# Performance work log

Measured on AMD Instinct MI355X. Metric: run time of the kernel, lower is better.

## Reference

```python
import jax, jax.numpy as jnp
import numpy as np

SIGMA = 0.002  # TreeEnergyLoss default; edge weight = exp(-||df||^2 / sigma)


def bilinear_resize(x, oh, ow):
    """F.interpolate(mode='bilinear', align_corners=False), no antialias. x: [B,C,H,W]."""
    B, C, H, W = x.shape
    if (H, W) == (oh, ow):
        return x
    def coords(o, n):
        s = (jnp.arange(o, dtype=jnp.float32) + 0.5) * (n / o) - 0.5
        s = jnp.clip(s, 0.0, n - 1.0)
        lo = jnp.floor(s).astype(jnp.int32)
        hi = jnp.minimum(lo + 1, n - 1)
        return lo, hi, s - lo.astype(jnp.float32)
    r0, r1, rf = coords(oh, H)
    c0, c1, cf = coords(ow, W)
    xr = x[:, :, r0, :] * (1.0 - rf)[None, None, :, None] + x[:, :, r1, :] * rf[None, None, :, None]
    return xr[:, :, :, c0] * (1.0 - cf) + xr[:, :, :, c1] * cf


def nearest_resize(x, oh, ow):
    B, C, H, W = x.shape
    if (H, W) == (oh, ow):
        return x
    ri = jnp.floor(jnp.arange(oh) * (H / oh)).astype(jnp.int32)
    ci = jnp.floor(jnp.arange(ow) * (W / ow)).astype(jnp.int32)
    return x[:, :, ri, :][:, :, :, ci]


def _mst_bfs_np(embed, H, W):
    """Kruskal MST on the 4-connected pixel grid (edge cost = squared L2 feature
    distance, as in MinimumSpanningTree(TreeFilter2D.norm2_distance)), then BFS
    order from vertex 0. embed: np [C,H,W]. Returns (sorted_index, sorted_parent)
    where sorted_parent is the BFS position of each vertex's parent."""
    V = H * W
    idx = np.arange(V).reshape(H, W)
    eu = np.concatenate([idx[:-1, :].ravel(), idx[:, :-1].ravel()])
    ev = np.concatenate([idx[1:, :].ravel(), idx[:, 1:].ravel()])
    f = embed.reshape(embed.shape[0], V)
    cost = ((f[:, eu] - f[:, ev]) ** 2).sum(0)
    parent = np.arange(V)
    def find(x):
        root = x
        while parent[root] != root:
            root = parent[root]
        while parent[x] != root:
            parent[x], x = root, parent[x]
        return root
    nbr = [[] for _ in range(V)]
    cnt = 0
    for e in np.argsort(cost, kind='stable'):
        u, v = int(eu[e]), int(ev[e])
        ru, rv = find(u), find(v)
        if ru != rv:
            parent[ru] = rv
            nbr[u].append(v)
            nbr[v].append(u)
            cnt += 1
            if cnt == V - 1:
                break
    sorted_index = np.empty(V, np.int32)
    sorted_parent = np.empty(V, np.int32)
    visited = np.zeros(V, bool)
    sorted_index[0] = 0; sorted_parent[0] = 0; visited[0] = True
    head, tail = 0, 1
    while head < tail:
        u = int(sorted_index[head])
        for v in nbr[u]:
            if not visited[v]:
                visited[v] = True
                sorted_index[tail] = v
                sorted_parent[tail] = head
                tail += 1
        head += 1
    return sorted_index, sorted_parent


def build_trees(embed):
    """embed: [B,C,H,W]. Host-side MST+BFS per batch element (torch.no_grad in original)."""
    e = np.asarray(jax.lax.stop_gradient(embed), dtype=np.float64)
    B, C, H, W = e.shape
    si, sp = zip(*[_mst_bfs_np(e[b], H, W) for b in range(B)])
    return jnp.asarray(np.stack(si)), jnp.asarray(np.stack(sp))


def _tree_filter_single(f, embed, sorted_index, sorted_parent):
    """Normalized tree filter: out_i = sum_j W_ij f_j / sum_j W_ij with
    W_ij = prod of exp(-||de||^2/sigma) along the unique tree path i->j.
    Computed exactly via bottom-up aggregation + top-down propagation in BFS order.
    f: [C,V], embed: [Ce,V]."""
    C, V = f.shape
    fs = f[:, sorted_index]                        # [C,V] features in BFS order
    es = embed[:, sorted_index]
    d = ((es - es[:, sorted_parent]) ** 2).sum(0)  # [V]; d[0]=0 (root self edge)
    w = jnp.exp(-d / SIGMA)                        # edge weight to parent
    # bottom-up: children have larger BFS index, so reverse order is valid.
    # extra ones-row carries the normalizer Z through the same recursion.
    S0 = jnp.concatenate([fs, jnp.ones((1, V), fs.dtype)], axis=0)
    def up(S, j):
        return S.at[:, sorted_parent[j]].add(w[j] * S[:, j]), None
    S, _ = jax.lax.scan(up, S0, jnp.arange(V - 1, 0, -1))
    # top-down: A_root = S_root; A_j = S_j + w_j * (A_parent - w_j * S_j)
    def down(A, j):
        p = sorted_parent[j]
        return A.at[:, j].set(S[:, j] + w[j] * (A[:, p] - w[j] * S[:, j])), None
    A0 = jnp.zeros_like(S).at[:, 0].set(S[:, 0])
    A, _ = jax.lax.scan(down, A0, jnp.arange(1, V))
    out_sorted = A[:C] / A[C]
    return jnp.zeros_like(f).at[:, sorted_index].set(out_sorted)


def tree_filter(feature, embed, si, sp):
    B, C, h, w = feature.shape
    out = jax.vmap(_tree_filter_single)(
        feature.reshape(B, C, h * w),
        embed.reshape(B, embed.shape[1], h * w), si, sp)
    return out.reshape(B, C, h, w)


def setup_inputs():
    key = jax.random.key(0)
    k1, k2, k3, k4 = jax.random.split(key, 4)
    preds = jax.random.normal(k1, (8, 21, 80, 80), jnp.float32)
    # scaled so exp(-||df||^2 / 0.002) gives non-degenerate edge weights
    low_feats = jax.random.uniform(k2, (8, 3, 80, 80), jnp.float32) * 0.02
    high_feats = jax.random.normal(k3, (8, 256, 80, 80), jnp.float32) * 0.002
    unlabeled_ROIs = jax.random.randint(k4, (8, 80, 80), 0, 2, dtype=jnp.int32)
    return {"preds": preds, "low_feats": low_feats,
            "high_feats": high_feats, "unlabeled_ROIs": unlabeled_ROIs}


def reference(preds, low_feats, high_feats, unlabeled_ROIs):
    B, C, h, w = preds.shape
    low = bilinear_resize(low_feats, h, w)  # under torch.no_grad in original
    roi = nearest_resize(unlabeled_ROIs[:, None].astype(jnp.float32), h, w)
    si_l, sp_l = build_trees(low)
    si_h, sp_h = build_trees(high_feats)
    prob = jax.nn.softmax(preds, axis=1)
    AS = tree_filter(prob, jax.lax.stop_gradient(low), si_l, sp_l)  # low-level tree
    AS = tree_filter(AS, high_feats, si_h, sp_h)                    # high-level tree
    N = roi.sum()
    loss = (roi * jnp.abs(prob - AS)).sum()
    return jnp.where(N > 0, loss / N, jnp.zeros((), preds.dtype))  # weight = 1.0
```

## Files before the change

kernel.cpp:

```cpp
#include <hip/hip_runtime.h>

#define BB 8
#define CP 21
#define CF 22
#define CLOW 3
#define CHIGH 256
#define WW 80
#define VV 6400
#define EVERT 6320
#define EE 12640
#define TT 16
#define SIGMA_F 0.002f
#define ROOT 3240

#define NE (VV - 1)
#define NA (2 * NE)
#define NILA 0xFFFFu
#define NB 200

__device__ __forceinline__ void edge_uv(int e, int& u, int& v) {
  if (e < EVERT) { u = e; v = e + WW; }
  else { int e2 = e - EVERT; int r = e2 / (WW - 1); int c = e2 - r * (WW - 1); u = r * WW + c; v = u + 1; }
}

__global__ void k_softmax(const float* __restrict__ preds, float* __restrict__ prob) {
  int i = blockIdx.x * blockDim.x + threadIdx.x;
  if (i >= BB * VV) return;
  int b = i / VV, v = i - b * VV;
  const float* p = preds + (size_t)b * CP * VV + v;
  float m = -1e30f;
  #pragma unroll
  for (int c = 0; c < CP; c++) m = fmaxf(m, p[c * VV]);
  float e[CP], s = 0.f;
  #pragma unroll
  for (int c = 0; c < CP; c++) { float x = expf(p[c * VV] - m); e[c] = x; s += x; }
  float inv = 1.f / s;
  float* o = prob + (size_t)b * CP * VV + v;
  #pragma unroll
  for (int c = 0; c < CP; c++) o[c * VV] = e[c] * inv;
}

__global__ void k_edgekey(const float* __restrict__ low, const float* __restrict__ high,
                          unsigned long long* __restrict__ ekey) {
  int i = blockIdx.x * blockDim.x + threadIdx.x;
  if (i >= TT * EE) return;
  int t = i / EE, e = i - t * EE;
  int u, v; edge_uv(e, u, v);
  double acc = 0.0;
  if (t < BB) {
    const float* emb = low + (size_t)t * CLOW * VV;
    for (int c = 0; c < CLOW; c++) { double d = (double)emb[c * VV + u] - (double)emb[c * VV + v]; acc += d * d; }
  } else {
    const float* emb = high + (size_t)(t - BB) * CHIGH * VV;
    for (int c = 0; c < CHIGH; c++) { double d = (double)emb[c * VV + u] - (double)emb[c * VV + v]; acc += d * d; }
  }
  unsigned long long bits = (unsigned long long)__double_as_longlong(acc);
  ekey[i] = (bits & ~0x3FFFULL) | (unsigned long long)e;
}

__global__ __launch_bounds__(1024) void k_msttree(const unsigned long long* __restrict__ ekey,
    int* __restrict__ mstU, int* __restrict__ mstV,
    int* __restrict__ ordG, int* __restrict__ spG,
    int* __restrict__ lpG, int* __restrict__ nlevG, float* __restrict__ wvp) {
  int t = blockIdx.x;
  const unsigned long long* key = ekey + (size_t)t * EE;
  int* mu = mstU + t * VV;
  int* mv = mstV + t * VV;
  int tid = threadIdx.x;
  const int nt = 1024;
  int lane = tid & 63, wid = tid >> 6;

  __shared__ alignas(16) char arena[144384];
  __shared__ int lasts, spackU, spackW, scenter, smaxd, changed, cnt, necnt;

  int* comp = (int*)(arena + 0);
  unsigned long long* bst = (unsigned long long*)(arena + 25600);
  unsigned short* tgtS = (unsigned short*)(arena + 76800);
  unsigned short* el0 = (unsigned short*)(arena + 89600);
  unsigned short* el1 = (unsigned short*)(arena + 114880);

  char* buf = arena;
  int* deg = (int*)(buf + 0);
  int* off = (int*)(buf + 25600);
  unsigned short* adjA = (unsigned short*)(buf + 51208);
  unsigned short* succ = (unsigned short*)(buf + 102408);
  int* pk0 = (int*)(buf + 0);
  int* pk1 = (int*)(buf + 51208);
  unsigned short* r_a = (unsigned short*)(buf + 102408);
  short* H = (short*)(buf + 51208);
  unsigned short* depthR = (unsigned short*)(buf + 76808);
  unsigned short* firstK = (unsigned short*)(buf + 89608);
  short* prefmin = (short*)(buf + 0);
  short* sufmin  = (short*)(buf + 25600);
  unsigned short* distU = (unsigned short*)(buf + 76808);
  unsigned short* parentS = (unsigned short*)(buf + 76808);
  int* lev = (int*)(buf + 0);
  int* cur = (int*)(buf + 25604);
  unsigned short* ordS = (unsigned short*)(buf + 51208);
  unsigned short* posS = (unsigned short*)(buf + 64008);
  int* part = (int*)(buf + 128016);
  short* tbl = (short*)(buf + 128272);
  unsigned short* dbuf2 = (unsigned short*)(buf + 131472);

  auto blockScanEx = [&](int s) -> int {
    int x = s;
    #pragma unroll
    for (int d = 1; d < 64; d <<= 1) { int o = __shfl_up(x, d); if (lane >= d) x += o; }
    if (lane == 63) part[wid] = x;
    __syncthreads();
    if (wid == 0) {
      int y = (lane < 16) ? part[lane] : 0;
      #pragma unroll
      for (int d = 1; d < 16; d <<= 1) { int o = __shfl_up(y, d); if (lane >= d) y += o; }
      if (lane < 16) part[lane] = y;
    }
    __syncthreads();
    int base = (wid > 0) ? part[wid - 1] : 0;
    return base + (x - s);
  };

  for (int v = tid; v < VV; v += nt) comp[v] = v;
  for (int e = tid; e < EE; e += nt) el0[e] = (unsigned short)e;
  if (tid == 0) cnt = 0;
  __syncthreads();
  {
    unsigned short* els = el0;
    unsigned short* eld = el1;
    int ecnt = EE;
    for (int round = 0; round < 48 && ecnt > 0; round++) {
      for (int v = tid; v < VV; v += nt) bst[v] = ~0ULL;
      if (tid == 0) { changed = 0; necnt = 0; }
      __syncthreads();
      for (int j = tid; j < ecnt; j += nt) {
        int e = els[j];
        int u, v; edge_uv(e, u, v);
        int cu = comp[u], cv = comp[v];
        if (cu != cv) { unsigned long long k = key[e]; atomicMin(&bst[cu], k); atomicMin(&bst[cv], k); }
      }
      __syncthreads();
      for (int c = tid; c < VV; c += nt) {
        unsigned short tg = (unsigned short)NILA;
        if (comp[c] == c) {
          unsigned long long k = bst[c];
          if (k != ~0ULL) {
            int e = (int)(k & 0x3FFFULL);
            int u, v; edge_uv(e, u, v);
            int cu = comp[u], cv = comp[v];
            tg = (unsigned short)((cu == c) ? cv : cu);
          }
        }
        tgtS[c] = tg;
      }
      __syncthreads();
      for (int c = tid; c < VV; c += nt) {
        int o = tgtS[c];
        if (o == (int)NILA) continue;
        unsigned long long k = bst[c];
        if (bst[o] == k && c < o) continue;
        comp[c] = o;
        int slot = atomicAdd(&cnt, 1);
        int e = (int)(k & 0x3FFFULL);
        int u, v; edge_uv(e, u, v);
        mu[slot] = u; mv[slot] = v;
        changed = 1;
      }
      __syncthreads();
      if (!changed) break;
      for (int v = tid; v < VV; v += nt) {
        int c = comp[v];
        int c2 = comp[c];
        if (c2 != c) {
          int r0 = c2;
          while (true) { int n = comp[r0]; if (n == r0) break; r0 = n; }
          comp[v] = r0;
        }
      }
      __syncthreads();
      for (int j = tid; j < ecnt; j += nt) {
        int e = els[j];
        int u, v; edge_uv(e, u, v);
        if (comp[u] != comp[v]) { int s = atomicAdd(&necnt, 1); eld[s] = (unsigned short)e; }
      }
      __syncthreads();
      ecnt = necnt;
      __syncthreads();
      unsigned short* tp = els; els = eld; eld = tp;
    }
  }
  __threadfence();
  __syncthreads();

  for (int v = tid; v < VV; v += nt) deg[v] = 0;
  __syncthreads();
  for (int e = tid; e < NE; e += nt) { atomicAdd(&deg[mu[e]], 1); atomicAdd(&deg[mv[e]], 1); }
  __syncthreads();
  {
    const int SCH = 7;
    int base = tid * SCH;
    int s = 0;
    #pragma unroll
    for (int k = 0; k < SCH; k++) { int v = base + k; if (v < VV) s += deg[v]; }
    int ex = blockScanEx(s);
    #pragma unroll
    for (int k = 0; k < SCH; k++) { int v = base + k; if (v < VV) { off[v] = ex; ex += deg[v]; } }
    if (tid == 1023) off[VV] = ex;
  }
  __syncthreads();
  for (int v = tid; v < VV; v += nt) deg[v] = off[v];
  __syncthreads();
  for (int e = tid; e < NE; e += nt) {
    int u = mu[e], v = mv[e];
    adjA[atomicAdd(&deg[u], 1)] = (unsigned short)(2 * e);
    adjA[atomicAdd(&deg[v], 1)] = (unsigned short)(2 * e + 1);
  }
  __syncthreads();
  for (int v = tid; v < VV; v += nt) {
    int b0 = off[v], dv = off[v + 1] - b0;
    for (int k = 0; k < dv; k++) {
      unsigned short a = adjA[b0 + k];
      unsigned short b = adjA[b0 + ((k + 1 == dv) ? 0 : k + 1)];
      succ[a ^ 1] = b;
    }
  }
  if (tid == 0) lasts = adjA[off[ROOT] + (off[ROOT + 1] - off[ROOT]) - 1] ^ 1;
  __syncthreads();
  if (tid == 0) succ[lasts] = (unsigned short)NILA;
  __syncthreads();
  for (int a = tid; a < NA; a += nt) {
    unsigned int n = succ[a];
    pk0[a] = ((n == NILA ? 0 : 1) << 16) | (int)n;
  }
  __syncthreads();
  {
    int* px = pk0;
    int* py = pk1;
    for (int rd = 0; rd < 14; rd++) {
      for (int a = tid; a < NA; a += nt) {
        int cur_ = px[a];
        int n = cur_ & 0xFFFF;
        if (n != (int)NILA) {
          int o = px[n];
          cur_ = (((cur_ >> 16) + (o >> 16)) << 16) | (o & 0xFFFF);
        }
        py[a] = cur_;
      }
      __syncthreads();
      int* tp = px; px = py; py = tp;
    }
    for (int a = tid; a < NA; a += nt) r_a[a] = (unsigned short)(pk0[a] >> 16);
  }
  __syncthreads();
  for (int a = tid; a < NA; a += nt) {
    int pa = NA - 1 - (int)r_a[a];
    int pb = NA - 1 - (int)r_a[a ^ 1];
    H[pa] = (pa < pb) ? (short)1 : (short)-1;
  }
  __syncthreads();
  {
    const int SCH = 13;
    int base = tid * SCH;
    int lim = base + SCH; if (lim > NA) lim = NA;
    int s = 0;
    for (int j = base; j < lim; j++) s += H[j];
    int run = blockScanEx(s);
    for (int j = base; j < lim; j++) { run += H[j]; H[j] = (short)run; }
  }
  __syncthreads();
  if (tid == 0) { spackU = 0; smaxd = 0; scenter = 0x7FFFFFFF; }
  __syncthreads();
  for (int a = tid; a < NA; a += nt) {
    int pa = NA - 1 - (int)r_a[a];
    int pb = NA - 1 - (int)r_a[a ^ 1];
    if (pa < pb) {
      int e = a >> 1;
      int head = (a & 1) ? mu[e] : mv[e];
      depthR[head] = (unsigned short)H[pa];
      firstK[head] = (unsigned short)(pa + 1);
    }
  }
  if (tid == 0) { depthR[ROOT] = 0; firstK[ROOT] = 0; }
  __syncthreads();
  {
    int loc = 0;
    for (int v = tid; v < VV; v += nt) { int p = ((int)depthR[v] << 13) | v; if (p > loc) loc = p; }
    #pragma unroll
    for (int d = 32; d > 0; d >>= 1) { int o = __shfl_down(loc, d); if (o > loc) loc = o; }
    if (lane == 0) atomicMax(&spackU, loc);
  }
  __syncthreads();
  {
    for (int seg = wid; seg < NB; seg += 16) {
      int p = seg * 64 + lane;
      int h = (p < NA) ? (int)H[p] : 32767;
      int hp = h;
      #pragma unroll
      for (int d = 1; d < 64; d <<= 1) { int o = __shfl_up(hp, d); if (lane >= d && o < hp) hp = o; }
      prefmin[p] = (short)hp;
      int hs = h;
      #pragma unroll
      for (int d = 1; d < 64; d <<= 1) { int o = __shfl_down(hs, d); if (lane + d < 64 && o < hs) hs = o; }
      sufmin[p] = (short)hs;
      if (lane == 0) tbl[seg] = (short)hs;
    }
  }
  __syncthreads();
  for (int k = 1; k < 8; k++) {
    short vv_ = 0;
    if (tid < NB) {
      int o = tid + (1 << (k - 1));
      short a = tbl[(k - 1) * NB + tid];
      short b2 = (o < NB) ? tbl[(k - 1) * NB + o] : (short)32767;
      vv_ = (a < b2) ? a : b2;
    }
    __syncthreads();
    if (tid < NB) tbl[k * NB + tid] = vv_;
    __syncthreads();
  }
  auto distq = [&](int K1, int K2) -> int {
    if (K1 == K2) return 0;
    int l = (K1 < K2 ? K1 : K2) - 1;
    int r = (K1 > K2 ? K1 : K2) - 1;
    int m = 32767;
    int l0 = l < 0 ? 0 : l;
    int bl = l0 >> 6, br = r >> 6;
    if (bl == br) {
      for (int p = l0; p <= r; p++) { int h = H[p]; if (h < m) m = h; }
    } else {
      int a = sufmin[l0], b2 = prefmin[r];
      m = a < b2 ? a : b2;
      int lo = bl + 1, hi = br - 1;
      if (lo <= hi) {
        int L = hi - lo + 1;
        int k = 31 - __builtin_clz(L);
        int c1 = tbl[k * NB + lo];
        int c2 = tbl[k * NB + hi - (1 << k) + 1];
        if (c1 < m) m = c1;
        if (c2 < m) m = c2;
      }
    }
    if (l < 0 && 0 < m) m = 0;
    int h1 = (K1 == 0) ? 0 : (int)H[K1 - 1];
    int h2 = (K2 == 0) ? 0 : (int)H[K2 - 1];
    return h1 + h2 - 2 * m;
  };
  int u = spackU & 0x1FFF;
  int Ku = firstK[u];
  if (tid == 0) spackW = 0;
  __syncthreads();
  {
    int loc = 0;
    for (int v = tid; v < VV; v += nt) {
      int d = distq(Ku, firstK[v]);
      distU[v] = (unsigned short)d;
      int p = (d << 13) | v;
      if (p > loc) loc = p;
    }
    #pragma unroll
    for (int d = 32; d > 0; d >>= 1) { int o = __shfl_down(loc, d); if (o > loc) loc = o; }
    if (lane == 0) atomicMax(&spackW, loc);
  }
  __syncthreads();
  int D = spackW >> 13;
  int w = spackW & 0x1FFF;
  int Kw = firstK[w];
  for (int v = tid; v < VV; v += nt) dbuf2[v] = (unsigned short)distq(Kw, firstK[v]);
  __syncthreads();
  {
    int half = D >> 1;
    for (int v = tid; v < VV; v += nt) {
      if ((int)distU[v] == half && (int)distU[v] + (int)dbuf2[v] == D) atomicMin(&scenter, v);
    }
  }
  __syncthreads();
  int cvert = (scenter == 0x7FFFFFFF) ? ROOT : scenter;
  int Kc = firstK[cvert];
  __syncthreads();
  {
    int loc = 0;
    for (int v = tid; v < VV; v += nt) {
      int d = distq(Kc, firstK[v]);
      dbuf2[v] = (unsigned short)d;
      if (d > loc) loc = d;
    }
    #pragma unroll
    for (int d = 32; d > 0; d >>= 1) { int o = __shfl_down(loc, d); if (o > loc) loc = o; }
    if (lane == 0) atomicMax(&smaxd, loc);
  }
  __syncthreads();
  int maxd = smaxd;
  int sTil = Kc;
  for (int a = tid; a < NA; a += nt) {
    int pa = NA - 1 - (int)r_a[a];
    int pb = NA - 1 - (int)r_a[a ^ 1];
    int pa2 = pa - sTil; if (pa2 < 0) pa2 += NA;
    int pb2 = pb - sTil; if (pb2 < 0) pb2 += NA;
    if (pa2 < pb2) {
      int e = a >> 1;
      int head = (a & 1) ? mu[e] : mv[e];
      int tail = (a & 1) ? mv[e] : mu[e];
      parentS[head] = (unsigned short)tail;
    }
  }
  if (tid == 0) parentS[cvert] = (unsigned short)cvert;
  __syncthreads();
  for (int d = tid; d <= VV; d += nt) lev[d] = 0;
  __syncthreads();
  for (int v = tid; v < VV; v += nt) atomicAdd(&lev[dbuf2[v]], 1);
  __syncthreads();
  {
    const int SCH = 7;
    int base = tid * SCH;
    int s = 0;
    #pragma unroll
    for (int k = 0; k < SCH; k++) { int d = base + k; if (d <= VV) s += lev[d]; }
    int ex = blockScanEx(s);
    #pragma unroll
    for (int k = 0; k < SCH; k++) {
      int d = base + k;
      if (d <= VV) {
        int st = ex;
        ex += lev[d];
        if (d < VV) cur[d] = st;
        lpG[t * (VV + 1) + d] = st;
      }
    }
  }
  __syncthreads();
  for (int v = tid; v < VV; v += nt) {
    int d = dbuf2[v];
    int slot = atomicAdd(&cur[d], 1);
    ordS[slot] = (unsigned short)v;
    posS[v] = (unsigned short)slot;
  }
  __syncthreads();
  for (int j = tid; j < VV; j += nt) {
    int v = ordS[j];
    int pv = parentS[v];
    ordG[t * VV + j] = v;
    spG[t * VV + j] = posS[pv];
    float wout;
    if (v == pv) {
      wout = 1.0f;
    } else {
      int a = v < pv ? v : pv;
      int diff = v < pv ? pv - v : v - pv;
      int e;
      if (diff == WW) e = a;
      else { int r = a / WW, c = a - r * WW; e = EVERT + r * (WW - 1) + c; }
      unsigned long long k = key[e];
      double cost = __longlong_as_double((long long)(k & ~0x3FFFULL));
      wout = expf(-(float)cost / SIGMA_F);
    }
    wvp[t * VV + j] = wout;
  }
  if (tid == 0) nlevG[t] = maxd + 1;
}

__global__ __launch_bounds__(512) void k_filter_pc(const float* __restrict__ Fsrc, float* __restrict__ Araw,
    const float* __restrict__ wvp, const int* __restrict__ ordG, const int* __restrict__ spG,
    const int* __restrict__ lpG, const int* __restrict__ nlevG, int treeBase) {
  int blk = blockIdx.x;
  int b = blk / CF, ch = blk - b * CF;
  int t = treeBase + b;
  __shared__ alignas(16) char arena[140816];
  float2* ab0 = (float2*)(arena);
  float2* ab1 = (float2*)(arena + 51200);
  float*  S   = (float*)(arena + 51200);
  float*  w   = (float*)(arena + 76800);
  unsigned short* sp0 = (unsigned short*)(arena + 102400);
  unsigned short* sp1 = (unsigned short*)(arena + 115200);
  unsigned short* lpS = (unsigned short*)(arena + 128000);
  const int* ord = ordG + t * VV;
  const int* spt = spG + t * VV;
  const float* wsrc = wvp + t * VV;
  const int* lp = lpG + t * (VV + 1);
  int tid = threadIdx.x;
  const int nt = 512;
  int NL = nlevG[t];
  for (int j = tid; j <= NL; j += nt) lpS[j] = (unsigned short)lp[j];
  const bool norm_in = (treeBase != 0);
  for (int j = tid; j < VV; j += nt) {
    sp0[j] = (unsigned short)spt[j];
    w[j] = wsrc[j];
    float val;
    if (ch < CP) {
      int v = ord[j];
      if (!norm_in) val = Fsrc[((size_t)b * CP + ch) * VV + v];
      else          val = Fsrc[((size_t)b * CF + ch) * VV + v] / Fsrc[((size_t)b * CF + CP) * VV + v];
    } else val = 1.0f;
    S[j] = val;
  }
  __syncthreads();
  if (tid < 64) {
    int s1 = lpS[NL];
    int s0 = lpS[NL - 1];
    for (int l = NL - 1; l >= 1; l--) {
      int s0n = (l > 1) ? (int)lpS[l - 1] : 0;
      for (int j = s0 + tid; j < s1; j += 64) {
        atomicAdd(&S[sp0[j]], w[j] * S[j]);
      }
      asm volatile("s_waitcnt lgkmcnt(0)" ::: "memory");
      __builtin_amdgcn_sched_barrier(0);
      s1 = s0; s0 = s0n;
    }
  }
  __syncthreads();
  for (int j = tid; j < VV; j += nt) {
    float wv = w[j];
    float a = (j == 0) ? 0.f : wv;
    float bv = (j == 0) ? S[0] : S[j] * (1.f - wv * wv);
    ab0[j] = make_float2(a, bv);
  }
  __syncthreads();
  int rounds = 0;
  { int d = 1; while (d < NL) { d <<= 1; rounds++; } }
  float2 *abs_ = ab0, *abd_ = ab1;
  unsigned short *ps_ = sp0, *pd_ = sp1;
  for (int r = 0; r < rounds; r++) {
    for (int j = tid; j < VV; j += nt) {
      float2 m = abs_[j];
      int p = ps_[j];
      float2 o = m;
      int pn = p;
      if (m.x != 0.f) {
        float2 mp = abs_[p];
        pn = ps_[p];
        o.x = m.x * mp.x;
        o.y = fmaf(m.x, mp.y, m.y);
      }
      abd_[j] = o;
      pd_[j] = (unsigned short)pn;
    }
    __syncthreads();
    float2* tf = abs_; abs_ = abd_; abd_ = tf;
    unsigned short* tu = ps_; ps_ = pd_; pd_ = tu;
  }
  float* Ob = Araw + ((size_t)b * CF + ch) * VV;
  for (int j = tid; j < VV; j += nt) Ob[ord[j]] = abs_[j].y;
}

__global__ void k_loss(const float* __restrict__ prob, const float* __restrict__ Araw2,
                       const int* __restrict__ roi, double* __restrict__ acc) {
  int i = blockIdx.x * blockDim.x + threadIdx.x;
  int tid = threadIdx.x;
  double s = 0.0, n = 0.0;
  if (i < BB * VV) {
    int b = i / VV, v = i - b * VV;
    if (roi[i] != 0) {
      n = 1.0;
      const float* pb = prob + (size_t)b * CP * VV + v;
      const float* ab = Araw2 + (size_t)b * CF * VV + v;
      float inv = 1.0f / ab[CP * VV];
      float ls = 0.f;
      #pragma unroll
      for (int c = 0; c < CP; c++) ls += fabsf(pb[c * VV] - ab[c * VV] * inv);
      s = (double)ls;
    }
  }
  __shared__ double rs[256], rn[256];
  rs[tid] = s; rn[tid] = n;
  __syncthreads();
  for (int d = 128; d > 0; d >>= 1) {
    if (tid < d) { rs[tid] += rs[tid + d]; rn[tid] += rn[tid + d]; }
    __syncthreads();
  }
  if (tid == 0) { atomicAdd(&acc[0], rs[0]); atomicAdd(&acc[1], rn[0]); }
}

__global__ void k_finalize(const double* __restrict__ acc, float* __restrict__ out) {
  out[0] = (acc[1] > 0.0) ? (float)(acc[0] / acc[1]) : 0.0f;
}

extern "C" void kernel_launch(void* const* d_in, const int* in_sizes, int n_in,
                              void* d_out, int out_size, void* d_ws, size_t ws_size,
                              hipStream_t stream) {
  const float* preds = (const float*)d_in[0];
  const float* low   = (const float*)d_in[1];
  const float* high  = (const float*)d_in[2];
  const int*   roi   = (const int*)d_in[3];
  float* out = (float*)d_out;

  char* w = (char*)d_ws;
  size_t off = 0;
  auto alloc = [&](size_t bytes) -> void* {
    void* p = w + off;
    off += (bytes + 255) & ~(size_t)255;
    return p;
  };
  float* prob  = (float*)alloc((size_t)BB * CP * VV * 4);
  float* Araw1 = (float*)alloc((size_t)BB * CF * VV * 4);
  float* Araw2 = (float*)alloc((size_t)BB * CF * VV * 4);
  unsigned long long* ekey = (unsigned long long*)alloc((size_t)TT * EE * 8);
  int* mstU = (int*)alloc((size_t)TT * VV * 4);
  int* mstV = (int*)alloc((size_t)TT * VV * 4);
  int* ordG = (int*)alloc((size_t)TT * VV * 4);
  int* spG  = (int*)alloc((size_t)TT * VV * 4);
  int* lpG  = (int*)alloc((size_t)TT * (VV + 1) * 4);
  int* nlev = (int*)alloc((size_t)TT * 4);
  float* wvp = (float*)alloc((size_t)TT * VV * 4);
  double* acc = (double*)alloc(16);

  hipMemsetAsync(acc, 0, 16, stream);

  k_softmax<<<(BB * VV + 255) / 256, 256, 0, stream>>>(preds, prob);
  k_edgekey<<<(TT * EE + 255) / 256, 256, 0, stream>>>(low, high, ekey);
  k_msttree<<<TT, 1024, 0, stream>>>(ekey, mstU, mstV, ordG, spG, lpG, nlev, wvp);
  k_filter_pc<<<BB * CF, 512, 0, stream>>>(prob,  Araw1, wvp, ordG, spG, lpG, nlev, 0);
  k_filter_pc<<<BB * CF, 512, 0, stream>>>(Araw1, Araw2, wvp, ordG, spG, lpG, nlev, BB);
  k_loss<<<(BB * VV + 255) / 256, 256, 0, stream>>>(prob, Araw2, roi, acc);
  k_finalize<<<1, 1, 0, stream>>>(acc, out);
}
```

Measured before the change: 301.1 us.

## Fold softmax into MST kernel, fuse finalize into loss, widen filter blocks

Softmax now runs as extra blocks of the MST kernel launch, so it uses the CUs left idle by the 16 MST blocks. The finalize kernel is removed: the last k_loss block, found with an atomic done-counter, writes the result. The filter kernel goes from 512 to 1024 threads per block to parallelise the per-level scans. This saves two launches and fills idle hardware, at the cost of more register pressure from the 1024-thread launch bound and extra code inside the MST kernel.

```diff
diff --git a/kernel.cpp b/kernel.cpp
--- a/kernel.cpp
+++ b/kernel.cpp
@@ -17,27 +17,11 @@
 #define NA (2 * NE)
 #define NILA 0xFFFFu
 #define NB 200
+#define SMB ((BB * VV + 255) / 256)
 
 __device__ __forceinline__ void edge_uv(int e, int& u, int& v) {
   if (e < EVERT) { u = e; v = e + WW; }
   else { int e2 = e - EVERT; int r = e2 / (WW - 1); int c = e2 - r * (WW - 1); u = r * WW + c; v = u + 1; }
-}
-
-__global__ void k_softmax(const float* __restrict__ preds, float* __restrict__ prob) {
-  int i = blockIdx.x * blockDim.x + threadIdx.x;
-  if (i >= BB * VV) return;
-  int b = i / VV, v = i - b * VV;
-  const float* p = preds + (size_t)b * CP * VV + v;
-  float m = -1e30f;
-  #pragma unroll
-  for (int c = 0; c < CP; c++) m = fmaxf(m, p[c * VV]);
-  float e[CP], s = 0.f;
-  #pragma unroll
-  for (int c = 0; c < CP; c++) { float x = expf(p[c * VV] - m); e[c] = x; s += x; }
-  float inv = 1.f / s;
-  float* o = prob + (size_t)b * CP * VV + v;
-  #pragma unroll
-  for (int c = 0; c < CP; c++) o[c * VV] = e[c] * inv;
 }
 
 __global__ void k_edgekey(const float* __restrict__ low, const float* __restrict__ high,
@@ -61,7 +45,26 @@
 __global__ __launch_bounds__(1024) void k_msttree(const unsigned long long* __restrict__ ekey,
     int* __restrict__ mstU, int* __restrict__ mstV,
     int* __restrict__ ordG, int* __restrict__ spG,
-    int* __restrict__ lpG, int* __restrict__ nlevG, float* __restrict__ wvp) {
+    int* __restrict__ lpG, int* __restrict__ nlevG, float* __restrict__ wvp,
+    const float* __restrict__ preds, float* __restrict__ prob) {
+  if (blockIdx.x >= TT) {
+    int i = (blockIdx.x - TT) * 1024 + threadIdx.x;
+    if (i < BB * VV) {
+      int b = i / VV, v = i - b * VV;
+      const float* p = preds + (size_t)b * CP * VV + v;
+      float m = -1e30f;
+      #pragma unroll
+      for (int c = 0; c < CP; c++) m = fmaxf(m, p[c * VV]);
+      float e[CP], s = 0.f;
+      #pragma unroll
+      for (int c = 0; c < CP; c++) { float x = expf(p[c * VV] - m); e[c] = x; s += x; }
+      float inv = 1.f / s;
+      float* o = prob + (size_t)b * CP * VV + v;
+      #pragma unroll
+      for (int c = 0; c < CP; c++) o[c * VV] = e[c] * inv;
+    }
+    return;
+  }
   int t = blockIdx.x;
   const unsigned long long* key = ekey + (size_t)t * EE;
   int* mu = mstU + t * VV;
@@ -456,7 +459,7 @@
   if (tid == 0) nlevG[t] = maxd + 1;
 }
 
-__global__ __launch_bounds__(512) void k_filter_pc(const float* __restrict__ Fsrc, float* __restrict__ Araw,
+__global__ __launch_bounds__(1024) void k_filter_pc(const float* __restrict__ Fsrc, float* __restrict__ Araw,
     const float* __restrict__ wvp, const int* __restrict__ ordG, const int* __restrict__ spG,
     const int* __restrict__ lpG, const int* __restrict__ nlevG, int treeBase) {
   int blk = blockIdx.x;
@@ -475,7 +478,7 @@
   const float* wsrc = wvp + t * VV;
   const int* lp = lpG + t * (VV + 1);
   int tid = threadIdx.x;
-  const int nt = 512;
+  const int nt = 1024;
   int NL = nlevG[t];
   for (int j = tid; j <= NL; j += nt) lpS[j] = (unsigned short)lp[j];
   const bool norm_in = (treeBase != 0);
@@ -540,7 +543,8 @@
 }
 
 __global__ void k_loss(const float* __restrict__ prob, const float* __restrict__ Araw2,
-                       const int* __restrict__ roi, double* __restrict__ acc) {
+                       const int* __restrict__ roi, double* __restrict__ acc,
+                       unsigned int* __restrict__ done, float* __restrict__ out) {
   int i = blockIdx.x * blockDim.x + threadIdx.x;
   int tid = threadIdx.x;
   double s = 0.0, n = 0.0;
@@ -558,17 +562,26 @@
     }
   }
   __shared__ double rs[256], rn[256];
+  __shared__ bool amLast;
   rs[tid] = s; rn[tid] = n;
   __syncthreads();
   for (int d = 128; d > 0; d >>= 1) {
     if (tid < d) { rs[tid] += rs[tid + d]; rn[tid] += rn[tid + d]; }
     __syncthreads();
   }
-  if (tid == 0) { atomicAdd(&acc[0], rs[0]); atomicAdd(&acc[1], rn[0]); }
-}
-
-__global__ void k_finalize(const double* __restrict__ acc, float* __restrict__ out) {
-  out[0] = (acc[1] > 0.0) ? (float)(acc[0] / acc[1]) : 0.0f;
+  if (tid == 0) {
+    atomicAdd(&acc[0], rs[0]);
+    atomicAdd(&acc[1], rn[0]);
+    __threadfence();
+    unsigned int prev = atomicAdd(done, 1u);
+    amLast = (prev == gridDim.x - 1);
+  }
+  __syncthreads();
+  if (amLast && tid == 0) {
+    __threadfence();
+    double ss = acc[0], nn = acc[1];
+    out[0] = (nn > 0.0) ? (float)(ss / nn) : 0.0f;
+  }
 }
 
 extern "C" void kernel_launch(void* const* d_in, const int* in_sizes, int n_in,
@@ -598,15 +611,15 @@
   int* lpG  = (int*)alloc((size_t)TT * (VV + 1) * 4);
   int* nlev = (int*)alloc((size_t)TT * 4);
   float* wvp = (float*)alloc((size_t)TT * VV * 4);
-  double* acc = (double*)alloc(16);
-
-  hipMemsetAsync(acc, 0, 16, stream);
-
-  k_softmax<<<(BB * VV + 255) / 256, 256, 0, stream>>>(preds, prob);
+  double* acc = (double*)alloc(32);
+
+  hipMemsetAsync(acc, 0, 32, stream);
+
+  const int nSoft = (BB * VV + 1023) / 1024;
   k_edgekey<<<(TT * EE + 255) / 256, 256, 0, stream>>>(low, high, ekey);
-  k_msttree<<<TT, 1024, 0, stream>>>(ekey, mstU, mstV, ordG, spG, lpG, nlev, wvp);
-  k_filter_pc<<<BB * CF, 512, 0, stream>>>(prob,  Araw1, wvp, ordG, spG, lpG, nlev, 0);
-  k_filter_pc<<<BB * CF, 512, 0, stream>>>(Araw1, Araw2, wvp, ordG, spG, lpG, nlev, BB);
-  k_loss<<<(BB * VV + 255) / 256, 256, 0, stream>>>(prob, Araw2, roi, acc);
-  k_finalize<<<1, 1, 0, stream>>>(acc, out);
+  k_msttree<<<TT + nSoft, 1024, 0, stream>>>(ekey, mstU, mstV, ordG, spG, lpG, nlev, wvp, preds, prob);
+  k_filter_pc<<<BB * CF, 1024, 0, stream>>>(prob,  Araw1, wvp, ordG, spG, lpG, nlev, 0);
+  k_filter_pc<<<BB * CF, 1024, 0, stream>>>(Araw1, Araw2, wvp, ordG, spG, lpG, nlev, BB);
+  k_loss<<<(BB * VV + 255) / 256, 256, 0, stream>>>(prob, Araw2, roi, acc,
+      (unsigned int*)(acc + 2), out);
 }
```

New measurement: 278.3 us. 1.08x faster.
